# Kernel tuning notes

Hardware: AMD Instinct MI355X
Metric: run time of the kernel (lower is better)

The kernel has to match this reference:

```python
import jax, jax.numpy as jnp
import numpy as np

B, N, C, K = 64, 32768, 2, 10   # batch, num predictions, num classes, padded GT slots (build_target default N=10)
VL = 1.0e6                      # 'very_large' sentinel from torch code
EPS = 1e-08
W_LOC = W_CLASS = W_CONF = 1.0


def setup_inputs() -> dict:
    key = jax.random.key(0)
    k1, k2, k3, k4, k5, k6, k7 = jax.random.split(key, 7)
    p_start = jax.random.normal(k1, (B, N), dtype=jnp.float32)
    p_end = jax.random.normal(k2, (B, N), dtype=jnp.float32)
    p_class_logits = jax.random.normal(k3, (B, N, C), dtype=jnp.float32)
    p_conf_logits = jax.random.normal(k4, (B, N), dtype=jnp.float32)
    # GT intervals in [0,1] (compared against sigmoid(pred)); class channel in {0,1}
    fs = jax.random.uniform(k5, (B, K), dtype=jnp.float32)
    fe = jnp.clip(fs + 0.2 * jax.random.uniform(k6, (B, K), dtype=jnp.float32), 0.0, 1.0)
    cls = jax.random.randint(k7, (B, K), 0, C).astype(jnp.float32)
    gt_boxes = jnp.stack([fs, fe, cls], axis=-1)  # (B, K, 3)
    return {'p_start': p_start, 'p_end': p_end, 'p_class_logits': p_class_logits,
            'p_conf_logits': p_conf_logits, 'gt_boxes': gt_boxes}


def _build_target(gt_boxes):
    fs, fe, cls = gt_boxes[..., 0], gt_boxes[..., 1], gt_boxes[..., 2]
    presence = (~(jnp.isnan(fs) | jnp.isnan(fe) | jnp.isnan(cls))).astype(jnp.float32)
    fs = jnp.nan_to_num(fs)
    fe = jnp.nan_to_num(fe)
    cls = jnp.nan_to_num(cls)
    onehot = jax.nn.one_hot(jnp.clip(cls.astype(jnp.int32), 0, C - 1), C, dtype=jnp.float32)
    return fs, fe, onehot, presence


def _match_and_losses(cost, ps, pe, pcl, pconf, fs, fe, onehot):
    # cost: (K, N); greedy one-to-one argmin matching with row/col masking.
    Kp, Np = cost.shape

    def step(c, _):
        flat = c.reshape(-1)
        idx = jnp.argmin(flat)
        val = flat[idx]
        row, col = idx // Np, idx % Np
        valid = val < VL / 2
        c = c.at[row, :].set(VL).at[:, col].set(VL)
        return c, (row, col, valid)

    _, (rows, cols, valids) = jax.lax.scan(step, jax.lax.stop_gradient(cost), None, length=Kp)
    vm = valids.astype(jnp.float32)  # (K,)

    sel_s = jax.nn.sigmoid(ps[cols])
    sel_e = jax.nn.sigmoid(pe[cols])
    gs, ge = fs[rows], fe[rows]
    loc = (sel_s - gs) ** 2 + (sel_e - ge) ** 2

    logits = pcl[cols]          # (K, C)
    y = onehot[rows]            # (K, C)
    bce = (y * jax.nn.softplus(-logits) + (1.0 - y) * jax.nn.softplus(logits)).sum(-1)

    # IoU target is computed from .item() values in torch -> constant (no grad)
    ss, se = jax.lax.stop_gradient(sel_s), jax.lax.stop_gradient(sel_e)
    gss, gse = jax.lax.stop_gradient(gs), jax.lax.stop_gradient(ge)
    a1, b1 = jnp.minimum(ss, se), jnp.maximum(ss, se)
    a2, b2 = jnp.minimum(gss, gse), jnp.maximum(gss, gse)
    inter = jnp.maximum(0.0, jnp.minimum(b1, b2) - jnp.maximum(a1, a2))
    union = jnp.maximum(EPS, jnp.maximum(b1, b2) - jnp.minimum(a1, a2))
    iou = inter / union
    conf = (jax.nn.sigmoid(pconf[cols]) - iou) ** 2

    return (loc * vm).sum(), (bce * vm).sum(), (conf * vm).sum(), vm.sum()


def reference(p_start, p_end, p_class_logits, p_conf_logits, gt_boxes):
    fs, fe, onehot, presence = _build_target(gt_boxes)  # (B,K), (B,K), (B,K,C), (B,K)
    ps_sig = jax.nn.sigmoid(p_start)
    pe_sig = jax.nn.sigmoid(p_end)
    # loc MSE cost: (B, K, N)
    loc = (ps_sig[:, None, :] - fs[:, :, None]) ** 2 + (pe_sig[:, None, :] - fe[:, :, None]) ** 2
    # class L2 cost without materializing (B,K,N,C): |a-b|^2 = |a|^2 - 2 a.b + |b|^2
    sc = jax.nn.sigmoid(p_class_logits)  # (B, N, C)
    class_l2 = ((sc ** 2).sum(-1)[:, None, :]
                - 2.0 * jnp.einsum('bnc,bkc->bkn', sc, onehot)
                + (onehot ** 2).sum(-1)[:, :, None])
    cost = loc + class_l2
    # invalid (absent) GT rows get sentinel cost so greedy skips them
    cost = jnp.where(presence[:, :, None] > 0, cost, VL)

    loc_s, cls_s, conf_s, m = jax.vmap(_match_and_losses)(
        cost, p_start, p_end, p_class_logits, p_conf_logits, fs, fe, onehot)

    total_m = m.sum()
    denom = total_m + EPS
    total = (W_LOC * loc_s.sum() + W_CLASS * cls_s.sum() + W_CONF * conf_s.sum()) / denom
    return jnp.where(total_m > 0, total, 0.0)
```

## Files before the change

kernel.cpp:

```cpp
#include <hip/hip_runtime.h>
#include <cfloat>
#include <cmath>

#define BB 64
#define NN 32768
#define CC 2
#define KK 10
#define S_SL 32
#define SLICE (NN / S_SL)
#define TPS 256
#define TPM 256
#define VLARGE 1.0e6
#define KEY_MAX 0xFFFFFFFFFFFFFFFFull
#define BND_MARGIN 1.0e-3

__device__ __forceinline__ double dsig(float x) { return 1.0 / (1.0 + exp(-(double)x)); }
__device__ __forceinline__ double dsoftplus(double x) {
    return fmax(x, 0.0) + log1p(exp(-fabs(x)));
}
__device__ __forceinline__ unsigned long long packkey(float v, int c) {
    return ((unsigned long long)__float_as_uint(v) << 32) | (unsigned int)c;
}
__device__ __forceinline__ void merge2(unsigned long long& a1, unsigned long long& a2,
                                       unsigned long long b1, unsigned long long b2) {
    unsigned long long lo = a1 < b1 ? a1 : b1;
    unsigned long long hi = a1 < b1 ? b1 : a1;
    unsigned long long mb = a2 < b2 ? a2 : b2;
    a2 = hi < mb ? hi : mb;
    a1 = lo;
}
__device__ __forceinline__ void colterms(float sraw, float eraw, float q0raw, float q1raw,
                                         float& s, float& e, float& u0, float& u1) {
    s = __fdividef(1.0f, 1.0f + __expf(-sraw));
    e = __fdividef(1.0f, 1.0f + __expf(-eraw));
    const float q0 = __fdividef(1.0f, 1.0f + __expf(-q0raw));
    const float q1 = __fdividef(1.0f, 1.0f + __expf(-q1raw));
    const float se2 = fmaf(s, s, e * e);
    const float t0 = q0 - 1.0f, t1 = q1 - 1.0f;
    u0 = se2 + fmaf(t0, t0, q1 * q1);
    u1 = se2 + fmaf(t1, t1, q0 * q0);
}
__device__ __forceinline__ float rowcost(float s, float e, float u0, float u1,
                                         float m0, float m1, float ckv, int cls, int pres) {
    float c = fmaf(m0, s, fmaf(m1, e, ((cls == 0) ? u0 : u1) + ckv));
    c = fmaxf(c, 0.0f);
    return pres ? c : (float)VLARGE;
}
__device__ __forceinline__ double eval64(const float* ps, const float* pe, const float* pc,
                                         double fs, double fe, int cls, int pres, int col) {
    if (!pres) return VLARGE;
    const double s  = dsig(ps[col]);
    const double e  = dsig(pe[col]);
    const double q0 = dsig(pc[2 * col]);
    const double q1 = dsig(pc[2 * col + 1]);
    const double d0 = s - fs, d1 = e - fe;
    const double sc = (cls == 0) ? q0 : q1;
    return d0 * d0 + d1 * d1 + (q0 * q0 + q1 * q1 - 2.0 * sc + 1.0);
}

__global__ __launch_bounds__(TPS)
void scan_kernel(const float* __restrict__ p_start, const float* __restrict__ p_end,
                 const float* __restrict__ p_cls, const float* __restrict__ gt,
                 ulonglong2* __restrict__ cand) {
    const int sl = blockIdx.x, b = blockIdx.y;
    const int tid = threadIdx.x, wv = tid >> 6, lane = tid & 63;
    const float2* ps2 = (const float2*)(p_start + (size_t)b * NN);
    const float2* pe2 = (const float2*)(p_end   + (size_t)b * NN);
    const float4* pc4 = (const float4*)(p_cls   + (size_t)b * NN * CC);

    float m0[KK], m1[KK], ck[KK]; int rcl[KK], rpres[KK];
    #pragma unroll
    for (int k = 0; k < KK; k++) {
        float f0 = gt[((size_t)b * KK + k) * 3 + 0];
        float f1 = gt[((size_t)b * KK + k) * 3 + 1];
        float f2 = gt[((size_t)b * KK + k) * 3 + 2];
        int pres = !(isnan(f0) || isnan(f1) || isnan(f2));
        if (isnan(f0)) f0 = 0.0f;
        if (isnan(f1)) f1 = 0.0f;
        if (isnan(f2)) f2 = 0.0f;
        int ci = (int)f2; ci = ci < 0 ? 0 : (ci > CC - 1 ? CC - 1 : ci);
        m0[k] = -2.0f * f0; m1[k] = -2.0f * f1;
        ck[k] = fmaf(f0, f0, f1 * f1);
        rcl[k] = ci; rpres[k] = pres;
    }

    float v1[KK], v2[KK]; int c1[KK], c2[KK];
    #pragma unroll
    for (int k = 0; k < KK; k++) { v1[k] = FLT_MAX; v2[k] = FLT_MAX; c1[k] = 0x7fffffff; c2[k] = 0x7fffffff; }

    const int base2 = sl * (SLICE / 2) + wv * 128;
    #pragma unroll
    for (int it = 0; it < 2; it++) {
        const int pidx = base2 + it * 64 + lane;
        const float2 sv = ps2[pidx];
        const float2 ev = pe2[pidx];
        const float4 cv = pc4[pidx];
        #pragma unroll
        for (int h = 0; h < 2; h++) {
            const int n = 2 * pidx + h;
            float s, e, u0, u1;
            colterms(h ? sv.y : sv.x, h ? ev.y : ev.x,
                     h ? cv.z : cv.x, h ? cv.w : cv.y, s, e, u0, u1);
            #pragma unroll
            for (int k = 0; k < KK; k++) {
                const float cost = rowcost(s, e, u0, u1, m0[k], m1[k], ck[k], rcl[k], rpres[k]);
                const bool lt1 = cost < v1[k], lt2 = cost < v2[k];
                v2[k] = lt2 ? (lt1 ? v1[k] : cost) : v2[k];
                c2[k] = lt2 ? (lt1 ? c1[k] : n)    : c2[k];
                v1[k] = lt1 ? cost : v1[k];
                c1[k] = lt1 ? n    : c1[k];
            }
        }
    }

    unsigned long long k1[KK], k2[KK];
    #pragma unroll
    for (int k = 0; k < KK; k++) { k1[k] = packkey(v1[k], c1[k]); k2[k] = packkey(v2[k], c2[k]); }
    #pragma unroll
    for (int off = 1; off < 64; off <<= 1) {
        #pragma unroll
        for (int k = 0; k < KK; k++) {
            unsigned long long o1 = __shfl_xor(k1[k], off, 64);
            unsigned long long o2 = __shfl_xor(k2[k], off, 64);
            merge2(k1[k], k2[k], o1, o2);
        }
    }
    __shared__ unsigned long long s1[4][KK], s2[4][KK];
    if (lane == 0) {
        #pragma unroll
        for (int k = 0; k < KK; k++) { s1[wv][k] = k1[k]; s2[wv][k] = k2[k]; }
    }
    __syncthreads();
    if (tid < KK) {
        unsigned long long a1 = s1[0][tid], a2 = s2[0][tid];
        #pragma unroll
        for (int w = 1; w < 4; w++) merge2(a1, a2, s1[w][tid], s2[w][tid]);
        ulonglong2 pk; pk.x = a1; pk.y = a2;
        cand[((size_t)b * S_SL + sl) * KK + tid] = pk;
    }
}

__global__ __launch_bounds__(TPM)
void match_kernel(const float* __restrict__ p_start, const float* __restrict__ p_end,
                  const float* __restrict__ p_cls, const float* __restrict__ p_conf,
                  const float* __restrict__ gt, const ulonglong2* __restrict__ cand,
                  double* __restrict__ partials, unsigned int* __restrict__ counter,
                  float* __restrict__ out, int out_size) {
    const int b = blockIdx.x, tid = threadIdx.x;
    const int j = tid & 63, wv = tid >> 6;
    const float* ps  = p_start + (size_t)b * NN;
    const float* pe  = p_end   + (size_t)b * NN;
    const float* pc  = p_cls   + (size_t)b * NN * CC;
    const float* pcf = p_conf  + (size_t)b * NN;

    __shared__ double l_cost[KK][64];
    __shared__ int    l_col[KK][64];
    __shared__ double l_bnd[KK][S_SL];
    __shared__ double gfs[KK], gfe[KK];
    __shared__ int    gcls[KK], gpres[KK];

    if (tid < KK) {
        float f0 = gt[((size_t)b * KK + tid) * 3 + 0];
        float f1 = gt[((size_t)b * KK + tid) * 3 + 1];
        float f2 = gt[((size_t)b * KK + tid) * 3 + 2];
        int pres = !(isnan(f0) || isnan(f1) || isnan(f2));
        if (isnan(f0)) f0 = 0.0f;
        if (isnan(f1)) f1 = 0.0f;
        if (isnan(f2)) f2 = 0.0f;
        int ci = (int)f2; ci = ci < 0 ? 0 : (ci > CC - 1 ? CC - 1 : ci);
        gfs[tid] = (double)f0; gfe[tid] = (double)f1;
        gcls[tid] = ci; gpres[tid] = pres;
    }
    __syncthreads();

    for (int idx = tid; idx < KK * 64; idx += TPM) {
        const int r = idx >> 6, jj = idx & 63, sl = jj >> 1;
        ulonglong2 pk = cand[((size_t)b * S_SL + sl) * KK + r];
        const unsigned long long key = (jj & 1) ? pk.y : pk.x;
        int c = (int)(unsigned int)(key & 0xffffffffull);
        if (c < 0 || c >= NN) c = 0;
        l_cost[r][jj] = eval64(ps, pe, pc, gfs[r], gfe[r], gcls[r], gpres[r], c);
        l_col[r][jj]  = c;
        if (jj & 1)
            l_bnd[r][sl] = (double)__uint_as_float((unsigned int)(key >> 32)) - BND_MARGIN;
    }
    __syncthreads();
    if (wv != 0) return;

    const int s_my = j >> 1;
    double val[KK]; int col[KK]; double bnd[KK];
    #pragma unroll
    for (int r = 0; r < KK; r++) {
        val[r] = l_cost[r][j]; col[r] = l_col[r][j]; bnd[r] = l_bnd[r][s_my];
    }

    unsigned act = (1u << KK) - 1;
    int cons[KK], prow[KK], pcolv[KK], pvalid[KK];
    #pragma unroll
    for (int r = 0; r < KK; r++) { cons[r] = -1; pvalid[r] = 0; prow[r] = 0; pcolv[r] = 0; }

    for (int step = 0; step < KK; step++) {
        double bv = DBL_MAX; int brow = 0x7fffffff, bcol = 0x7fffffff;
        for (int guard = 0; guard < 64; guard++) {
            double lv = DBL_MAX; int lr = 0x7fffffff, lc = 0x7fffffff;
            #pragma unroll
            for (int r = 0; r < KK; r++) {
                if (!((act >> r) & 1)) continue;
                const int pcold = __shfl(col[r], j ^ 1, 64);
                const bool mine  = (col[r] >= 0);
                const bool bound = !mine && (pcold < 0) && ((j & 1) == 0);
                const double v = mine ? val[r] : (bound ? bnd[r] : DBL_MAX);
                const int    c = mine ? col[r] : (bound ? (-2 - s_my) : 0x7fffffff);
                if (v < lv || (v == lv && (r < lr || (r == lr && c < lc)))) {
                    lv = v; lr = r; lc = c;
                }
            }
            #pragma unroll
            for (int off = 1; off < 64; off <<= 1) {
                const double ov = __shfl_xor(lv, off, 64);
                const int   orr = __shfl_xor(lr, off, 64);
                const int   oc  = __shfl_xor(lc, off, 64);
                if (ov < lv || (ov == lv && (orr < lr || (orr == lr && oc < lc)))) {
                    lv = ov; lr = orr; lc = oc;
                }
            }
            bv = lv; brow = lr; bcol = lc;
            if (bcol >= 0 || bv == DBL_MAX) break;

            const int ss = -2 - bcol;
            const float ffs = (float)gfs[brow], ffe = (float)gfe[brow];
            const int   cb  = gcls[brow], pb = gpres[brow];
            const float m0b = -2.0f * ffs, m1b = -2.0f * ffe;
            const float ckb = fmaf(ffs, ffs, ffe * ffe);
            unsigned long long r1 = KEY_MAX, r2 = KEY_MAX;
            const int cbase = ss * SLICE;
            for (int t = j; t < SLICE; t += 64) {
                const int n = cbase + t;
                bool used = false;
                #pragma unroll
                for (int u = 0; u < KK; u++) used |= (cons[u] == n);
                float s, e, u0, u1;
                colterms(ps[n], pe[n], pc[2 * n], pc[2 * n + 1], s, e, u0, u1);
                const float cst = rowcost(s, e, u0, u1, m0b, m1b, ckb, cb, pb);
                const unsigned long long kk = used ? KEY_MAX : packkey(cst, n);
                if (kk < r2) { if (kk < r1) { r2 = r1; r1 = kk; } else { r2 = kk; } }
            }
            #pragma unroll
            for (int off = 1; off < 64; off <<= 1) {
                const unsigned long long o1 = __shfl_xor(r1, off, 64);
                const unsigned long long o2 = __shfl_xor(r2, off, 64);
                merge2(r1, r2, o1, o2);
            }
            int cA = (int)(unsigned int)(r1 & 0xffffffffull);
            int cB = (int)(unsigned int)(r2 & 0xffffffffull);
            if (cA < 0 || cA >= NN) cA = 0;
            if (cB < 0 || cB >= NN) cB = 0;
            const double vA = (r1 == KEY_MAX) ? DBL_MAX
                : eval64(ps, pe, pc, gfs[brow], gfe[brow], cb, pb, cA);
            const double vB = (r2 == KEY_MAX) ? DBL_MAX
                : eval64(ps, pe, pc, gfs[brow], gfe[brow], cb, pb, cB);
            const double nb = (r2 == KEY_MAX) ? DBL_MAX
                : (double)__uint_as_float((unsigned int)(r2 >> 32)) - BND_MARGIN;
            #pragma unroll
            for (int r = 0; r < KK; r++) {
                if (r != brow) continue;
                if (j == 2 * ss)     { val[r] = vA; col[r] = (r1 == KEY_MAX) ? -1 : cA; }
                if (j == 2 * ss + 1) { val[r] = vB; col[r] = (r2 == KEY_MAX) ? -1 : cB; }
                if (s_my == ss) bnd[r] = nb;
            }
        }

        prow[step]   = brow;
        pcolv[step]  = bcol;
        pvalid[step] = (bv < VLARGE * 0.5) && (bcol >= 0) && (brow < KK);
        cons[step]   = (bcol >= 0) ? bcol : -1;
        if (brow < KK) act &= ~(1u << brow);
        else break;

        if (bcol >= 0) {
            #pragma unroll
            for (int r = 0; r < KK; r++)
                if (col[r] == bcol) col[r] = -1;
        }
    }

    double loss = 0.0, m = 0.0;
    if (j < KK && pvalid[j]) {
        const int r = prow[j], cidx = pcolv[j];
        const double ss = dsig(ps[cidx]);
        const double se = dsig(pe[cidx]);
        const double gs = gfs[r], ge = gfe[r];
        const double d0 = ss - gs, d1 = se - ge;
        double acc = d0 * d0 + d1 * d1;

        const double l0 = (double)pc[2 * cidx];
        const double l1 = (double)pc[2 * cidx + 1];
        const double y0 = (gcls[r] == 0) ? 1.0 : 0.0;
        const double y1 = 1.0 - y0;
        acc += y0 * dsoftplus(-l0) + (1.0 - y0) * dsoftplus(l0)
             + y1 * dsoftplus(-l1) + (1.0 - y1) * dsoftplus(l1);

        const double a1 = fmin(ss, se), b1 = fmax(ss, se);
        const double a2 = fmin(gs, ge), b2 = fmax(gs, ge);
        const double inter = fmax(0.0, fmin(b1, b2) - fmax(a1, a2));
        const double uni   = fmax(1e-8, fmax(b1, b2) - fmin(a1, a2));
        const double iou   = inter / uni;
        const double dcf   = dsig(pcf[cidx]) - iou;
        acc += dcf * dcf;
        loss = acc; m = 1.0;
    }
    #pragma unroll
    for (int off = 1; off < 64; off <<= 1) {
        loss += __shfl_xor(loss, off, 64);
        m    += __shfl_xor(m, off, 64);
    }
    if (j == 0) { partials[b * 2 + 0] = loss; partials[b * 2 + 1] = m; }

    __threadfence();
    int ticket = 0;
    if (j == 0) ticket = (int)atomicAdd(counter, 1u);
    ticket = __shfl(ticket, 0, 64);
    if (ticket == BB - 1) {
        __threadfence();
        for (int i = j; i < out_size; i += 64) out[i] = 0.0f;
        double s = partials[j * 2 + 0];
        double mm = partials[j * 2 + 1];
        #pragma unroll
        for (int off = 1; off < 64; off <<= 1) {
            s  += __shfl_xor(s, off, 64);
            mm += __shfl_xor(mm, off, 64);
        }
        if (j == 0) {
            const double total = s / (mm + 1e-8);
            out[0] = (float)(mm > 0.0 ? total : 0.0);
        }
    }
}

extern "C" void kernel_launch(void* const* d_in, const int* in_sizes, int n_in,
                              void* d_out, int out_size, void* d_ws, size_t ws_size,
                              hipStream_t stream) {
    const float* p_start = (const float*)d_in[0];
    const float* p_end   = (const float*)d_in[1];
    const float* p_cls   = (const float*)d_in[2];
    const float* p_conf  = (const float*)d_in[3];
    const float* gt      = (const float*)d_in[4];

    const size_t cand_bytes = (size_t)BB * S_SL * KK * sizeof(ulonglong2);
    const size_t part_bytes = (size_t)BB * 2 * sizeof(double);
    ulonglong2*   cand     = (ulonglong2*)d_ws;
    double*       partials = (double*)((char*)d_ws + cand_bytes);
    unsigned int* counter  = (unsigned int*)((char*)d_ws + cand_bytes + part_bytes);

    hipMemsetAsync(counter, 0, sizeof(unsigned int), stream);
    scan_kernel<<<dim3(S_SL, BB), TPS, 0, stream>>>(p_start, p_end, p_cls, gt, cand);
    match_kernel<<<BB, TPM, 0, stream>>>(p_start, p_end, p_cls, p_conf, gt, cand,
                                         partials, counter, (float*)d_out, out_size);
}
```

Before: 165.0 us.

## Fuse scan and match kernels using per-batch last-block ticket

```diff
diff --git a/kernel.cpp b/kernel.cpp
--- a/kernel.cpp
+++ b/kernel.cpp
@@ -8,8 +8,9 @@
 #define KK 10
 #define S_SL 32
 #define SLICE (NN / S_SL)
-#define TPS 256
-#define TPM 256
+#define WPB 4
+#define TPB 256
+#define NBLK_PER_B (S_SL / WPB)
 #define VLARGE 1.0e6
 #define KEY_MAX 0xFFFFFFFFFFFFFFFFull
 #define BND_MARGIN 1.0e-3
@@ -41,10 +42,9 @@
     u1 = se2 + fmaf(t1, t1, q0 * q0);
 }
 __device__ __forceinline__ float rowcost(float s, float e, float u0, float u1,
-                                         float m0, float m1, float ckv, int cls, int pres) {
+                                         float m0, float m1, float ckv, int cls) {
     float c = fmaf(m0, s, fmaf(m1, e, ((cls == 0) ? u0 : u1) + ckv));
-    c = fmaxf(c, 0.0f);
-    return pres ? c : (float)VLARGE;
+    return fmaxf(c, 0.0f);
 }
 __device__ __forceinline__ double eval64(const float* ps, const float* pe, const float* pc,
                                          double fs, double fe, int cls, int pres, int col) {
@@ -58,17 +58,38 @@
     return d0 * d0 + d1 * d1 + (q0 * q0 + q1 * q1 - 2.0 * sc + 1.0);
 }
 
-__global__ __launch_bounds__(TPS)
-void scan_kernel(const float* __restrict__ p_start, const float* __restrict__ p_end,
-                 const float* __restrict__ p_cls, const float* __restrict__ gt,
-                 ulonglong2* __restrict__ cand) {
-    const int sl = blockIdx.x, b = blockIdx.y;
+__global__ __launch_bounds__(TPB)
+void fused_kernel(const float* __restrict__ p_start, const float* __restrict__ p_end,
+                  const float* __restrict__ p_cls, const float* __restrict__ p_conf,
+                  const float* __restrict__ gt, ulonglong2* __restrict__ cand,
+                  double* __restrict__ partials, unsigned int* __restrict__ batch_cnt,
+                  unsigned int* __restrict__ counter, float* __restrict__ out, int out_size) {
+    const int sx = blockIdx.x, b = blockIdx.y;
     const int tid = threadIdx.x, wv = tid >> 6, lane = tid & 63;
-    const float2* ps2 = (const float2*)(p_start + (size_t)b * NN);
-    const float2* pe2 = (const float2*)(p_end   + (size_t)b * NN);
-    const float4* pc4 = (const float4*)(p_cls   + (size_t)b * NN * CC);
-
-    float m0[KK], m1[KK], ck[KK]; int rcl[KK], rpres[KK];
+    const int sl = sx * WPB + wv;
+    const float* ps  = p_start + (size_t)b * NN;
+    const float* pe  = p_end   + (size_t)b * NN;
+    const float* pc  = p_cls   + (size_t)b * NN * CC;
+    const float* pcf = p_conf  + (size_t)b * NN;
+    const float2* ps2 = (const float2*)ps;
+    const float2* pe2 = (const float2*)pe;
+    const float4* pc4 = (const float4*)pc;
+
+    __shared__ double l_cost[KK][64];
+    __shared__ int    l_col[KK][64];
+    __shared__ double l_bnd[KK][S_SL];
+    __shared__ double gfs[KK], gfe[KK];
+    __shared__ int    gcls[KK], gpres[KK];
+    __shared__ int    s_ticket;
+
+    float2 SV[8], EV[8]; float4 CV[8];
+    #pragma unroll
+    for (int it = 0; it < 8; it++) {
+        const int pidx = sl * (SLICE / 2) + it * 64 + lane;
+        SV[it] = ps2[pidx]; EV[it] = pe2[pidx]; CV[it] = pc4[pidx];
+    }
+
+    float m0[KK], m1[KK], ck[KK]; int rcl[KK];
     #pragma unroll
     for (int k = 0; k < KK; k++) {
         float f0 = gt[((size_t)b * KK + k) * 3 + 0];
@@ -80,30 +101,25 @@
         if (isnan(f2)) f2 = 0.0f;
         int ci = (int)f2; ci = ci < 0 ? 0 : (ci > CC - 1 ? CC - 1 : ci);
         m0[k] = -2.0f * f0; m1[k] = -2.0f * f1;
-        ck[k] = fmaf(f0, f0, f1 * f1);
-        rcl[k] = ci; rpres[k] = pres;
+        ck[k] = fmaf(f0, f0, f1 * f1) + (pres ? 0.0f : (float)VLARGE);
+        rcl[k] = ci;
     }
 
     float v1[KK], v2[KK]; int c1[KK], c2[KK];
     #pragma unroll
     for (int k = 0; k < KK; k++) { v1[k] = FLT_MAX; v2[k] = FLT_MAX; c1[k] = 0x7fffffff; c2[k] = 0x7fffffff; }
 
-    const int base2 = sl * (SLICE / 2) + wv * 128;
-    #pragma unroll
-    for (int it = 0; it < 2; it++) {
-        const int pidx = base2 + it * 64 + lane;
-        const float2 sv = ps2[pidx];
-        const float2 ev = pe2[pidx];
-        const float4 cv = pc4[pidx];
+    #pragma unroll
+    for (int it = 0; it < 8; it++) {
         #pragma unroll
         for (int h = 0; h < 2; h++) {
-            const int n = 2 * pidx + h;
+            const int n = 2 * (sl * (SLICE / 2) + it * 64 + lane) + h;
             float s, e, u0, u1;
-            colterms(h ? sv.y : sv.x, h ? ev.y : ev.x,
-                     h ? cv.z : cv.x, h ? cv.w : cv.y, s, e, u0, u1);
+            colterms(h ? SV[it].y : SV[it].x, h ? EV[it].y : EV[it].x,
+                     h ? CV[it].z : CV[it].x, h ? CV[it].w : CV[it].y, s, e, u0, u1);
             #pragma unroll
             for (int k = 0; k < KK; k++) {
-                const float cost = rowcost(s, e, u0, u1, m0[k], m1[k], ck[k], rcl[k], rpres[k]);
+                const float cost = rowcost(s, e, u0, u1, m0[k], m1[k], ck[k], rcl[k]);
                 const bool lt1 = cost < v1[k], lt2 = cost < v2[k];
                 v2[k] = lt2 ? (lt1 ? v1[k] : cost) : v2[k];
                 c2[k] = lt2 ? (lt1 ? c1[k] : n)    : c2[k];
@@ -125,39 +141,20 @@
             merge2(k1[k], k2[k], o1, o2);
         }
     }
-    __shared__ unsigned long long s1[4][KK], s2[4][KK];
     if (lane == 0) {
         #pragma unroll
-        for (int k = 0; k < KK; k++) { s1[wv][k] = k1[k]; s2[wv][k] = k2[k]; }
-    }
+        for (int k = 0; k < KK; k++) {
+            ulonglong2 pk; pk.x = k1[k]; pk.y = k2[k];
+            cand[((size_t)b * S_SL + sl) * KK + k] = pk;
+        }
+    }
+
+    __threadfence();
     __syncthreads();
-    if (tid < KK) {
-        unsigned long long a1 = s1[0][tid], a2 = s2[0][tid];
-        #pragma unroll
-        for (int w = 1; w < 4; w++) merge2(a1, a2, s1[w][tid], s2[w][tid]);
-        ulonglong2 pk; pk.x = a1; pk.y = a2;
-        cand[((size_t)b * S_SL + sl) * KK + tid] = pk;
-    }
-}
-
-__global__ __launch_bounds__(TPM)
-void match_kernel(const float* __restrict__ p_start, const float* __restrict__ p_end,
-                  const float* __restrict__ p_cls, const float* __restrict__ p_conf,
-                  const float* __restrict__ gt, const ulonglong2* __restrict__ cand,
-                  double* __restrict__ partials, unsigned int* __restrict__ counter,
-                  float* __restrict__ out, int out_size) {
-    const int b = blockIdx.x, tid = threadIdx.x;
-    const int j = tid & 63, wv = tid >> 6;
-    const float* ps  = p_start + (size_t)b * NN;
-    const float* pe  = p_end   + (size_t)b * NN;
-    const float* pc  = p_cls   + (size_t)b * NN * CC;
-    const float* pcf = p_conf  + (size_t)b * NN;
-
-    __shared__ double l_cost[KK][64];
-    __shared__ int    l_col[KK][64];
-    __shared__ double l_bnd[KK][S_SL];
-    __shared__ double gfs[KK], gfe[KK];
-    __shared__ int    gcls[KK], gpres[KK];
+    if (tid == 0) s_ticket = (int)atomicAdd(&batch_cnt[b], 1u);
+    __syncthreads();
+    if (s_ticket != NBLK_PER_B - 1) return;
+    __threadfence();
 
     if (tid < KK) {
         float f0 = gt[((size_t)b * KK + tid) * 3 + 0];
@@ -173,20 +170,21 @@
     }
     __syncthreads();
 
-    for (int idx = tid; idx < KK * 64; idx += TPM) {
-        const int r = idx >> 6, jj = idx & 63, sl = jj >> 1;
-        ulonglong2 pk = cand[((size_t)b * S_SL + sl) * KK + r];
+    for (int idx = tid; idx < KK * 64; idx += TPB) {
+        const int r = idx >> 6, jj = idx & 63, sli = jj >> 1;
+        ulonglong2 pk = cand[((size_t)b * S_SL + sli) * KK + r];
         const unsigned long long key = (jj & 1) ? pk.y : pk.x;
         int c = (int)(unsigned int)(key & 0xffffffffull);
         if (c < 0 || c >= NN) c = 0;
         l_cost[r][jj] = eval64(ps, pe, pc, gfs[r], gfe[r], gcls[r], gpres[r], c);
         l_col[r][jj]  = c;
         if (jj & 1)
-            l_bnd[r][sl] = (double)__uint_as_float((unsigned int)(key >> 32)) - BND_MARGIN;
+            l_bnd[r][sli] = (double)__uint_as_float((unsigned int)(key >> 32)) - BND_MARGIN;
     }
     __syncthreads();
     if (wv != 0) return;
 
+    const int j = lane;
     const int s_my = j >> 1;
     double val[KK]; int col[KK]; double bnd[KK];
     #pragma unroll
@@ -231,7 +229,7 @@
             const float ffs = (float)gfs[brow], ffe = (float)gfe[brow];
             const int   cb  = gcls[brow], pb = gpres[brow];
             const float m0b = -2.0f * ffs, m1b = -2.0f * ffe;
-            const float ckb = fmaf(ffs, ffs, ffe * ffe);
+            const float ckb = fmaf(ffs, ffs, ffe * ffe) + (pb ? 0.0f : (float)VLARGE);
             unsigned long long r1 = KEY_MAX, r2 = KEY_MAX;
             const int cbase = ss * SLICE;
             for (int t = j; t < SLICE; t += 64) {
@@ -241,7 +239,7 @@
                 for (int u = 0; u < KK; u++) used |= (cons[u] == n);
                 float s, e, u0, u1;
                 colterms(ps[n], pe[n], pc[2 * n], pc[2 * n + 1], s, e, u0, u1);
-                const float cst = rowcost(s, e, u0, u1, m0b, m1b, ckb, cb, pb);
+                const float cst = rowcost(s, e, u0, u1, m0b, m1b, ckb, cb);
                 const unsigned long long kk = used ? KEY_MAX : packkey(cst, n);
                 if (kk < r2) { if (kk < r1) { r2 = r1; r1 = kk; } else { r2 = kk; } }
             }
@@ -348,12 +346,13 @@
 
     const size_t cand_bytes = (size_t)BB * S_SL * KK * sizeof(ulonglong2);
     const size_t part_bytes = (size_t)BB * 2 * sizeof(double);
-    ulonglong2*   cand     = (ulonglong2*)d_ws;
-    double*       partials = (double*)((char*)d_ws + cand_bytes);
-    unsigned int* counter  = (unsigned int*)((char*)d_ws + cand_bytes + part_bytes);
-
-    hipMemsetAsync(counter, 0, sizeof(unsigned int), stream);
-    scan_kernel<<<dim3(S_SL, BB), TPS, 0, stream>>>(p_start, p_end, p_cls, gt, cand);
-    match_kernel<<<BB, TPM, 0, stream>>>(p_start, p_end, p_cls, p_conf, gt, cand,
-                                         partials, counter, (float*)d_out, out_size);
-}
+    ulonglong2*   cand      = (ulonglong2*)d_ws;
+    double*       partials  = (double*)((char*)d_ws + cand_bytes);
+    unsigned int* batch_cnt = (unsigned int*)((char*)d_ws + cand_bytes + part_bytes);
+    unsigned int* counter   = batch_cnt + BB;
+
+    hipMemsetAsync(batch_cnt, 0, (BB + 1) * sizeof(unsigned int), stream);
+    fused_kernel<<<dim3(NBLK_PER_B, BB), TPB, 0, stream>>>(
+        p_start, p_end, p_cls, p_conf, gt, cand, partials, batch_cnt, counter,
+        (float*)d_out, out_size);
+}
```

New measurement: 191.0 us. 15.7% more time.

## Pack candidate keys into 32-bit with truncated cost and local column index

Applied to the files above, without the earlier changes.

```diff
diff --git a/kernel.cpp b/kernel.cpp
--- a/kernel.cpp
+++ b/kernel.cpp
@@ -6,26 +6,27 @@
 #define NN 32768
 #define CC 2
 #define KK 10
-#define S_SL 32
+#define S_SL 64
 #define SLICE (NN / S_SL)
-#define TPS 256
 #define TPM 256
 #define VLARGE 1.0e6
-#define KEY_MAX 0xFFFFFFFFFFFFFFFFull
+#define KEY32_MAX 0xFFFFFFFFu
+#define VMASK 0xFFFFFC00u
+#define CMASK 0x3FFu
 #define BND_MARGIN 1.0e-3
 
 __device__ __forceinline__ double dsig(float x) { return 1.0 / (1.0 + exp(-(double)x)); }
 __device__ __forceinline__ double dsoftplus(double x) {
     return fmax(x, 0.0) + log1p(exp(-fabs(x)));
 }
-__device__ __forceinline__ unsigned long long packkey(float v, int c) {
-    return ((unsigned long long)__float_as_uint(v) << 32) | (unsigned int)c;
-}
-__device__ __forceinline__ void merge2(unsigned long long& a1, unsigned long long& a2,
-                                       unsigned long long b1, unsigned long long b2) {
-    unsigned long long lo = a1 < b1 ? a1 : b1;
-    unsigned long long hi = a1 < b1 ? b1 : a1;
-    unsigned long long mb = a2 < b2 ? a2 : b2;
+__device__ __forceinline__ float rdfl_f(float x) {
+    return __int_as_float(__builtin_amdgcn_readfirstlane(__float_as_int(x)));
+}
+__device__ __forceinline__ void merge2_32(unsigned& a1, unsigned& a2,
+                                          unsigned b1, unsigned b2) {
+    unsigned lo = a1 < b1 ? a1 : b1;
+    unsigned hi = a1 < b1 ? b1 : a1;
+    unsigned mb = a2 < b2 ? a2 : b2;
     a2 = hi < mb ? hi : mb;
     a1 = lo;
 }
@@ -41,10 +42,9 @@
     u1 = se2 + fmaf(t1, t1, q0 * q0);
 }
 __device__ __forceinline__ float rowcost(float s, float e, float u0, float u1,
-                                         float m0, float m1, float ckv, int cls, int pres) {
+                                         float m0, float m1, float ckv, int cls) {
     float c = fmaf(m0, s, fmaf(m1, e, ((cls == 0) ? u0 : u1) + ckv));
-    c = fmaxf(c, 0.0f);
-    return pres ? c : (float)VLARGE;
+    return fmaxf(c, 0.0f);
 }
 __device__ __forceinline__ double eval64(const float* ps, const float* pe, const float* pc,
                                          double fs, double fe, int cls, int pres, int col) {
@@ -58,17 +58,24 @@
     return d0 * d0 + d1 * d1 + (q0 * q0 + q1 * q1 - 2.0 * sc + 1.0);
 }
 
-__global__ __launch_bounds__(TPS)
+__global__ __launch_bounds__(64)
 void scan_kernel(const float* __restrict__ p_start, const float* __restrict__ p_end,
                  const float* __restrict__ p_cls, const float* __restrict__ gt,
-                 ulonglong2* __restrict__ cand) {
-    const int sl = blockIdx.x, b = blockIdx.y;
-    const int tid = threadIdx.x, wv = tid >> 6, lane = tid & 63;
+                 uint2* __restrict__ cand) {
+    const int sl = blockIdx.x, b = blockIdx.y, lane = threadIdx.x;
     const float2* ps2 = (const float2*)(p_start + (size_t)b * NN);
     const float2* pe2 = (const float2*)(p_end   + (size_t)b * NN);
     const float4* pc4 = (const float4*)(p_cls   + (size_t)b * NN * CC);
 
-    float m0[KK], m1[KK], ck[KK]; int rcl[KK], rpres[KK];
+    float2 SV[4], EV[4]; float4 CV[4];
+    const int base2 = sl * (SLICE / 2);
+    #pragma unroll
+    for (int it = 0; it < 4; it++) {
+        const int pidx = base2 + it * 64 + lane;
+        SV[it] = ps2[pidx]; EV[it] = pe2[pidx]; CV[it] = pc4[pidx];
+    }
+
+    float m0[KK], m1[KK], ck[KK]; int rcl[KK];
     #pragma unroll
     for (int k = 0; k < KK; k++) {
         float f0 = gt[((size_t)b * KK + k) * 3 + 0];
@@ -79,71 +86,58 @@
         if (isnan(f1)) f1 = 0.0f;
         if (isnan(f2)) f2 = 0.0f;
         int ci = (int)f2; ci = ci < 0 ? 0 : (ci > CC - 1 ? CC - 1 : ci);
-        m0[k] = -2.0f * f0; m1[k] = -2.0f * f1;
-        ck[k] = fmaf(f0, f0, f1 * f1);
-        rcl[k] = ci; rpres[k] = pres;
-    }
-
-    float v1[KK], v2[KK]; int c1[KK], c2[KK];
-    #pragma unroll
-    for (int k = 0; k < KK; k++) { v1[k] = FLT_MAX; v2[k] = FLT_MAX; c1[k] = 0x7fffffff; c2[k] = 0x7fffffff; }
-
-    const int base2 = sl * (SLICE / 2) + wv * 128;
-    #pragma unroll
-    for (int it = 0; it < 2; it++) {
-        const int pidx = base2 + it * 64 + lane;
-        const float2 sv = ps2[pidx];
-        const float2 ev = pe2[pidx];
-        const float4 cv = pc4[pidx];
+        m0[k] = rdfl_f(-2.0f * f0);
+        m1[k] = rdfl_f(-2.0f * f1);
+        ck[k] = rdfl_f(fmaf(f0, f0, f1 * f1) + (pres ? 0.0f : (float)VLARGE));
+        rcl[k] = __builtin_amdgcn_readfirstlane(ci);
+    }
+
+    unsigned k1[KK], k2[KK];
+    #pragma unroll
+    for (int k = 0; k < KK; k++) { k1[k] = KEY32_MAX; k2[k] = KEY32_MAX; }
+
+    #pragma unroll
+    for (int it = 0; it < 4; it++) {
         #pragma unroll
         for (int h = 0; h < 2; h++) {
-            const int n = 2 * pidx + h;
+            const unsigned colLocal = 2u * (it * 64 + lane) + h;
             float s, e, u0, u1;
-            colterms(h ? sv.y : sv.x, h ? ev.y : ev.x,
-                     h ? cv.z : cv.x, h ? cv.w : cv.y, s, e, u0, u1);
+            colterms(h ? SV[it].y : SV[it].x, h ? EV[it].y : EV[it].x,
+                     h ? CV[it].z : CV[it].x, h ? CV[it].w : CV[it].y, s, e, u0, u1);
             #pragma unroll
             for (int k = 0; k < KK; k++) {
-                const float cost = rowcost(s, e, u0, u1, m0[k], m1[k], ck[k], rcl[k], rpres[k]);
-                const bool lt1 = cost < v1[k], lt2 = cost < v2[k];
-                v2[k] = lt2 ? (lt1 ? v1[k] : cost) : v2[k];
-                c2[k] = lt2 ? (lt1 ? c1[k] : n)    : c2[k];
-                v1[k] = lt1 ? cost : v1[k];
-                c1[k] = lt1 ? n    : c1[k];
-            }
-        }
-    }
-
-    unsigned long long k1[KK], k2[KK];
-    #pragma unroll
-    for (int k = 0; k < KK; k++) { k1[k] = packkey(v1[k], c1[k]); k2[k] = packkey(v2[k], c2[k]); }
+                const float cost = rowcost(s, e, u0, u1, m0[k], m1[k], ck[k], rcl[k]);
+                const unsigned key = (__float_as_uint(cost) & VMASK) | colLocal;
+                if (key < k2[k]) {
+                    if (key < k1[k]) { k2[k] = k1[k]; k1[k] = key; }
+                    else             { k2[k] = key; }
+                }
+            }
+        }
+    }
+
     #pragma unroll
     for (int off = 1; off < 64; off <<= 1) {
         #pragma unroll
         for (int k = 0; k < KK; k++) {
-            unsigned long long o1 = __shfl_xor(k1[k], off, 64);
-            unsigned long long o2 = __shfl_xor(k2[k], off, 64);
-            merge2(k1[k], k2[k], o1, o2);
-        }
-    }
-    __shared__ unsigned long long s1[4][KK], s2[4][KK];
-    if (lane == 0) {
-        #pragma unroll
-        for (int k = 0; k < KK; k++) { s1[wv][k] = k1[k]; s2[wv][k] = k2[k]; }
-    }
-    __syncthreads();
-    if (tid < KK) {
-        unsigned long long a1 = s1[0][tid], a2 = s2[0][tid];
-        #pragma unroll
-        for (int w = 1; w < 4; w++) merge2(a1, a2, s1[w][tid], s2[w][tid]);
-        ulonglong2 pk; pk.x = a1; pk.y = a2;
-        cand[((size_t)b * S_SL + sl) * KK + tid] = pk;
+            const unsigned o1 = __shfl_xor(k1[k], off, 64);
+            const unsigned o2 = __shfl_xor(k2[k], off, 64);
+            merge2_32(k1[k], k2[k], o1, o2);
+        }
+    }
+    #pragma unroll
+    for (int k = 0; k < KK; k++) {
+        if (lane == k) {
+            uint2 pk; pk.x = k1[k]; pk.y = k2[k];
+            cand[((size_t)b * S_SL + sl) * KK + k] = pk;
+        }
     }
 }
 
 __global__ __launch_bounds__(TPM)
 void match_kernel(const float* __restrict__ p_start, const float* __restrict__ p_end,
                   const float* __restrict__ p_cls, const float* __restrict__ p_conf,
-                  const float* __restrict__ gt, const ulonglong2* __restrict__ cand,
+                  const float* __restrict__ gt, const uint2* __restrict__ cand,
                   double* __restrict__ partials, unsigned int* __restrict__ counter,
                   float* __restrict__ out, int out_size) {
     const int b = blockIdx.x, tid = threadIdx.x;
@@ -153,8 +147,8 @@
     const float* pc  = p_cls   + (size_t)b * NN * CC;
     const float* pcf = p_conf  + (size_t)b * NN;
 
-    __shared__ double l_cost[KK][64];
-    __shared__ int    l_col[KK][64];
+    __shared__ double l_cost[KK][2 * S_SL];
+    __shared__ int    l_col[KK][2 * S_SL];
     __shared__ double l_bnd[KK][S_SL];
     __shared__ double gfs[KK], gfe[KK];
     __shared__ int    gcls[KK], gpres[KK];
@@ -173,25 +167,26 @@
     }
     __syncthreads();
 
-    for (int idx = tid; idx < KK * 64; idx += TPM) {
-        const int r = idx >> 6, jj = idx & 63, sl = jj >> 1;
-        ulonglong2 pk = cand[((size_t)b * S_SL + sl) * KK + r];
-        const unsigned long long key = (jj & 1) ? pk.y : pk.x;
-        int c = (int)(unsigned int)(key & 0xffffffffull);
+    for (int idx = tid; idx < KK * 2 * S_SL; idx += TPM) {
+        const int r = idx >> 7, jj = idx & 127, sl = jj >> 1;
+        uint2 pk = cand[((size_t)b * S_SL + sl) * KK + r];
+        const unsigned key = (jj & 1) ? pk.y : pk.x;
+        int c = sl * SLICE + (int)(key & CMASK);
         if (c < 0 || c >= NN) c = 0;
         l_cost[r][jj] = eval64(ps, pe, pc, gfs[r], gfe[r], gcls[r], gpres[r], c);
         l_col[r][jj]  = c;
         if (jj & 1)
-            l_bnd[r][sl] = (double)__uint_as_float((unsigned int)(key >> 32)) - BND_MARGIN;
+            l_bnd[r][sl] = (double)__uint_as_float(key & VMASK) - BND_MARGIN;
     }
     __syncthreads();
     if (wv != 0) return;
 
-    const int s_my = j >> 1;
-    double val[KK]; int col[KK]; double bnd[KK];
+    double v0[KK], v1v[KK], bnd[KK]; int c0[KK], c1v[KK];
     #pragma unroll
     for (int r = 0; r < KK; r++) {
-        val[r] = l_cost[r][j]; col[r] = l_col[r][j]; bnd[r] = l_bnd[r][s_my];
+        v0[r] = l_cost[r][2 * j];     c0[r]  = l_col[r][2 * j];
+        v1v[r] = l_cost[r][2 * j + 1]; c1v[r] = l_col[r][2 * j + 1];
+        bnd[r] = l_bnd[r][j];
     }
 
     unsigned act = (1u << KK) - 1;
@@ -206,13 +201,13 @@
             #pragma unroll
             for (int r = 0; r < KK; r++) {
                 if (!((act >> r) & 1)) continue;
-                const int pcold = __shfl(col[r], j ^ 1, 64);
-                const bool mine  = (col[r] >= 0);
-                const bool bound = !mine && (pcold < 0) && ((j & 1) == 0);
-                const double v = mine ? val[r] : (bound ? bnd[r] : DBL_MAX);
-                const int    c = mine ? col[r] : (bound ? (-2 - s_my) : 0x7fffffff);
-                if (v < lv || (v == lv && (r < lr || (r == lr && c < lc)))) {
-                    lv = v; lr = r; lc = c;
+                const bool a0 = (c0[r] >= 0), a1 = (c1v[r] >= 0);
+                double va = DBL_MAX; int ca = 0x7fffffff;
+                if (a0) { va = v0[r]; ca = c0[r]; }
+                if (a1 && (v1v[r] < va || (v1v[r] == va && c1v[r] < ca))) { va = v1v[r]; ca = c1v[r]; }
+                if (!a0 && !a1 && bnd[r] < DBL_MAX) { va = bnd[r]; ca = -2 - j; }
+                if (va < lv || (va == lv && (r < lr || (r == lr && ca < lc)))) {
+                    lv = va; lr = r; lc = ca;
                 }
             }
             #pragma unroll
@@ -231,8 +226,8 @@
             const float ffs = (float)gfs[brow], ffe = (float)gfe[brow];
             const int   cb  = gcls[brow], pb = gpres[brow];
             const float m0b = -2.0f * ffs, m1b = -2.0f * ffe;
-            const float ckb = fmaf(ffs, ffs, ffe * ffe);
-            unsigned long long r1 = KEY_MAX, r2 = KEY_MAX;
+            const float ckb = fmaf(ffs, ffs, ffe * ffe) + (pb ? 0.0f : (float)VLARGE);
+            unsigned q1 = KEY32_MAX, q2 = KEY32_MAX;
             const int cbase = ss * SLICE;
             for (int t = j; t < SLICE; t += 64) {
                 const int n = cbase + t;
@@ -241,32 +236,34 @@
                 for (int u = 0; u < KK; u++) used |= (cons[u] == n);
                 float s, e, u0, u1;
                 colterms(ps[n], pe[n], pc[2 * n], pc[2 * n + 1], s, e, u0, u1);
-                const float cst = rowcost(s, e, u0, u1, m0b, m1b, ckb, cb, pb);
-                const unsigned long long kk = used ? KEY_MAX : packkey(cst, n);
-                if (kk < r2) { if (kk < r1) { r2 = r1; r1 = kk; } else { r2 = kk; } }
+                const float cst = rowcost(s, e, u0, u1, m0b, m1b, ckb, cb);
+                const unsigned kk = used ? KEY32_MAX : ((__float_as_uint(cst) & VMASK) | (unsigned)t);
+                if (kk < q2) { if (kk < q1) { q2 = q1; q1 = kk; } else { q2 = kk; } }
             }
             #pragma unroll
             for (int off = 1; off < 64; off <<= 1) {
-                const unsigned long long o1 = __shfl_xor(r1, off, 64);
-                const unsigned long long o2 = __shfl_xor(r2, off, 64);
-                merge2(r1, r2, o1, o2);
-            }
-            int cA = (int)(unsigned int)(r1 & 0xffffffffull);
-            int cB = (int)(unsigned int)(r2 & 0xffffffffull);
+                const unsigned o1 = __shfl_xor(q1, off, 64);
+                const unsigned o2 = __shfl_xor(q2, off, 64);
+                merge2_32(q1, q2, o1, o2);
+            }
+            int cA = cbase + (int)(q1 & CMASK);
+            int cB = cbase + (int)(q2 & CMASK);
             if (cA < 0 || cA >= NN) cA = 0;
             if (cB < 0 || cB >= NN) cB = 0;
-            const double vA = (r1 == KEY_MAX) ? DBL_MAX
+            const double vA = (q1 == KEY32_MAX) ? DBL_MAX
                 : eval64(ps, pe, pc, gfs[brow], gfe[brow], cb, pb, cA);
-            const double vB = (r2 == KEY_MAX) ? DBL_MAX
+            const double vB = (q2 == KEY32_MAX) ? DBL_MAX
                 : eval64(ps, pe, pc, gfs[brow], gfe[brow], cb, pb, cB);
-            const double nb = (r2 == KEY_MAX) ? DBL_MAX
-                : (double)__uint_as_float((unsigned int)(r2 >> 32)) - BND_MARGIN;
+            const double nb = (q2 == KEY32_MAX) ? DBL_MAX
+                : (double)__uint_as_float(q2 & VMASK) - BND_MARGIN;
             #pragma unroll
             for (int r = 0; r < KK; r++) {
                 if (r != brow) continue;
-                if (j == 2 * ss)     { val[r] = vA; col[r] = (r1 == KEY_MAX) ? -1 : cA; }
-                if (j == 2 * ss + 1) { val[r] = vB; col[r] = (r2 == KEY_MAX) ? -1 : cB; }
-                if (s_my == ss) bnd[r] = nb;
+                if (j == ss) {
+                    v0[r]  = vA; c0[r]  = (q1 == KEY32_MAX) ? -1 : cA;
+                    v1v[r] = vB; c1v[r] = (q2 == KEY32_MAX) ? -1 : cB;
+                    bnd[r] = nb;
+                }
             }
         }
 
@@ -279,8 +276,10 @@
 
         if (bcol >= 0) {
             #pragma unroll
-            for (int r = 0; r < KK; r++)
-                if (col[r] == bcol) col[r] = -1;
+            for (int r = 0; r < KK; r++) {
+                if (c0[r] == bcol)  { c0[r] = -1;  v0[r]  = DBL_MAX; }
+                if (c1v[r] == bcol) { c1v[r] = -1; v1v[r] = DBL_MAX; }
+            }
         }
     }
 
@@ -346,14 +345,14 @@
     const float* p_conf  = (const float*)d_in[3];
     const float* gt      = (const float*)d_in[4];
 
-    const size_t cand_bytes = (size_t)BB * S_SL * KK * sizeof(ulonglong2);
+    const size_t cand_bytes = (size_t)BB * S_SL * KK * sizeof(uint2);
     const size_t part_bytes = (size_t)BB * 2 * sizeof(double);
-    ulonglong2*   cand     = (ulonglong2*)d_ws;
+    uint2*        cand     = (uint2*)d_ws;
     double*       partials = (double*)((char*)d_ws + cand_bytes);
     unsigned int* counter  = (unsigned int*)((char*)d_ws + cand_bytes + part_bytes);
 
     hipMemsetAsync(counter, 0, sizeof(unsigned int), stream);
-    scan_kernel<<<dim3(S_SL, BB), TPS, 0, stream>>>(p_start, p_end, p_cls, gt, cand);
+    scan_kernel<<<dim3(S_SL, BB), 64, 0, stream>>>(p_start, p_end, p_cls, gt, cand);
     match_kernel<<<BB, TPM, 0, stream>>>(p_start, p_end, p_cls, p_conf, gt, cand,
                                          partials, counter, (float*)d_out, out_size);
 }
```

Measured after the change: 144.4 us. 1.14x faster.
